# Performance work log

Hardware: AMD Instinct MI355X
Metric: run time of the kernel (lower is better)

Reference implementation:

```python
import jax, jax.numpy as jnp
import numpy as np

B, Q, T, H, V = 8, 1, 2048, 512, 32000


def setup_inputs() -> dict:
    key = jax.random.key(0)
    k0, k1, k2, k3, k4 = jax.random.split(key, 5)
    s1 = 1.0 / np.sqrt(2 * H)
    return {
        "input_embeds": jax.random.normal(k0, (B, Q, H), dtype=jnp.float32),
        "target_embeds": jax.random.normal(k1, (B, T, H), dtype=jnp.float32),
        "input_mask": jnp.ones((B, T), dtype=jnp.float32),
        # MLP params: l1 Linear(2H->H, bias), l2 Linear(H->1, no bias)
        "w1": (jax.random.normal(k2, (H, 2 * H), dtype=jnp.float32) * s1),
        "b1": jnp.zeros((H,), dtype=jnp.float32),
        "w2": (jax.random.normal(k3, (H,), dtype=jnp.float32) * (1.0 / np.sqrt(H))),
        # decoder: Linear(H->V, no bias) -> weight [V, H]
        "decoder_weight": (jax.random.normal(k4, (V, H), dtype=jnp.float32) * 0.02),
    }


def reference(input_embeds, target_embeds, input_mask, w1, b1, w2, decoder_weight):
    h = w1.shape[0]
    # l1(cat(q, t)) == q @ W1q^T + t @ W1t^T + b1  (split first linear)
    w1q, w1t = w1[:, :h], w1[:, h:]
    q_proj = jnp.einsum('bqh,kh->bqk', input_embeds, w1q)        # [B,Q,H]
    t_proj = jnp.einsum('bth,kh->btk', target_embeds, w1t)       # [B,T,H]
    # pairwise query x target MLP scoring
    ht = jax.nn.relu(q_proj[:, :, None, :] + t_proj[:, None, :, :] + b1)  # [B,Q,T,H]
    repair_logits = jnp.einsum('bqtk,k->bqt', ht, w2)             # [B,Q,T]
    # _mask: mask*logits - 1000*(1-mask); mask [B,T] -> [B,1,T]
    mask = input_mask[:, None, :]
    repair_logits = mask * repair_logits - 1000.0 * (1.0 - mask)
    # decoder branch: query x vocab-row MLP scoring
    d_proj = jnp.einsum('vh,kh->vk', decoder_weight, w1t)         # [V,H]
    hd = jax.nn.relu(q_proj[:, :, None, :] + d_proj[None, None, :, :] + b1)  # [B,Q,V,H]
    decoder_logits = jnp.einsum('bqvk,k->bqv', hd, w2)            # [B,Q,V]
    out = jnp.concatenate([decoder_logits, repair_logits], axis=2)  # [B,Q,V+T]
    return jnp.squeeze(out, axis=1)  # Q == 1 -> [B, V+T]
```

## Files before the change

kernel.cpp:

```cpp
#include <hip/hip_runtime.h>

#define Hdim 512
#define Bdim 8
#define Tdim 2048
#define Vdim 32000
#define OUTW (Vdim + Tdim)
#define DEC_TILES (Vdim / 128)
#define REP_TILES ((Bdim * Tdim) / 128)
#define NTILES (DEC_TILES + REP_TILES)
#define PROWS (Vdim + Bdim * Tdim)

typedef __attribute__((ext_vector_type(8))) short short8;
typedef __attribute__((ext_vector_type(16))) float f32x16;

__device__ __forceinline__ unsigned bfr(float f) {
    union { float f; unsigned u; } x; x.f = f;
    return (x.u + 0x7FFFu + ((x.u >> 16) & 1u)) >> 16;
}
__device__ __forceinline__ float lo16f(unsigned u) { return __uint_as_float(u << 16); }
__device__ __forceinline__ float hi16f(unsigned u) { return __uint_as_float(u & 0xffff0000u); }

#define N8_DEC (Vdim * Hdim / 8)
#define N8_TGT (Bdim * Tdim * Hdim / 8)
#define N8_W1  (Hdim * 1024 / 8)
#define N8_ALL (N8_DEC + N8_TGT + N8_W1)
#define CVT_BLOCKS (N8_ALL / 256)
#define QP_BLOCKS (Bdim * Hdim / 4)

__global__ __launch_bounds__(256) void prep_kernel(
    const float* __restrict__ dec, const float* __restrict__ tgt,
    const float* __restrict__ w1, const float* __restrict__ x,
    const float* __restrict__ b1,
    unsigned short* __restrict__ decbf, unsigned short* __restrict__ tgtbf,
    unsigned short* __restrict__ w1bf, float* __restrict__ qp)
{
    const int bid = blockIdx.x;
    if (bid < CVT_BLOCKS) {
        int i = bid * 256 + threadIdx.x;
        const float* src; unsigned short* dst; int j;
        if (i < N8_DEC)                { src = dec; dst = decbf; j = i; }
        else if (i < N8_DEC + N8_TGT)  { src = tgt; dst = tgtbf; j = i - N8_DEC; }
        else                           { src = w1;  dst = w1bf;  j = i - N8_DEC - N8_TGT; }
        const float4* s = (const float4*)src + (size_t)j * 2;
        float4 v0 = s[0], v1 = s[1];
        uint4 o;
        o.x = bfr(v0.x) | (bfr(v0.y) << 16);
        o.y = bfr(v0.z) | (bfr(v0.w) << 16);
        o.z = bfr(v1.x) | (bfr(v1.y) << 16);
        o.w = bfr(v1.z) | (bfr(v1.w) << 16);
        ((uint4*)dst)[j] = o;
    } else {
        const int widx = (bid - CVT_BLOCKS) * 4 + (threadIdx.x >> 6);
        const int lane = threadIdx.x & 63;
        const int b = widx >> 9, k = widx & 511;
        const float4* xr = (const float4*)(x + b * Hdim);
        const float4* wr = (const float4*)(w1 + (size_t)k * 1024);
        float4 x0 = xr[lane * 2], x1 = xr[lane * 2 + 1];
        float4 w0 = wr[lane * 2], w1v = wr[lane * 2 + 1];
        float s = x0.x * w0.x + x0.y * w0.y + x0.z * w0.z + x0.w * w0.w
                + x1.x * w1v.x + x1.y * w1v.y + x1.z * w1v.z + x1.w * w1v.w;
#pragma unroll
        for (int off = 32; off > 0; off >>= 1) s += __shfl_down(s, off);
        if (lane == 0) qp[b * Hdim + k] = s + b1[k];
    }
}

__global__ __launch_bounds__(256, 4) void gemm_kernel(
    const unsigned short* __restrict__ Adec,
    const unsigned short* __restrict__ Atgt,
    const unsigned short* __restrict__ Wbf,
    unsigned short* __restrict__ P)
{
    __shared__ struct { unsigned short A[128][64]; unsigned short W[128][64]; } u;

    const int tid  = threadIdx.x;
    const int lane = tid & 63;
    const int w    = tid >> 6;

    const int mt = blockIdx.x >> 2;
    const int n0 = (blockIdx.x & 3) << 7;
    const bool is_dec = (mt < DEC_TILES);
    const int m0 = (is_dec ? mt : mt - DEC_TILES) << 7;
    const unsigned short* __restrict__ A = is_dec ? Adec : Atgt;
    const int base = is_dec ? m0 : Vdim + m0;

    const int sr = lane >> 3;
    const int sc = (lane & 7) ^ sr;
    const unsigned short* gA = A   + (size_t)(m0 + w * 32 + sr) * 512  + sc * 8;
    const unsigned short* gW = Wbf + (size_t)(n0 + w * 32 + sr) * 1024 + 512 + sc * 8;

    f32x16 acc00, acc01, acc10, acc11;
#pragma unroll
    for (int i = 0; i < 16; ++i) { acc00[i] = 0.f; acc01[i] = 0.f; acc10[i] = 0.f; acc11[i] = 0.f; }

    const int wm  = (w & 1) << 6;
    const int wn  = (w >> 1) << 6;
    const int l31 = lane & 31;
    const int kh  = lane >> 5;

    for (int h0 = 0; h0 < Hdim; h0 += 64) {
        __syncthreads();
#pragma unroll
        for (int i = 0; i < 4; ++i) {
            __builtin_amdgcn_global_load_lds(
                (const __attribute__((address_space(1))) unsigned int*)(gA + i * 8 * 512),
                (__attribute__((address_space(3))) unsigned int*)(&u.A[w * 32 + i * 8][0]),
                16, 0, 0);
            __builtin_amdgcn_global_load_lds(
                (const __attribute__((address_space(1))) unsigned int*)(gW + i * 8 * 1024),
                (__attribute__((address_space(3))) unsigned int*)(&u.W[w * 32 + i * 8][0]),
                16, 0, 0);
        }
        gA += 64; gW += 64;
        __syncthreads();
#pragma unroll
        for (int s = 0; s < 4; ++s) {
            const int g  = s * 2 + kh;
            const int ca = ((g ^ (l31 & 7)) << 3);
            short8 a0 = *(const short8*)&u.A[wm + l31][ca];
            short8 a1 = *(const short8*)&u.A[wm + l31 + 32][ca];
            short8 b0 = *(const short8*)&u.W[wn + l31][ca];
            short8 b1 = *(const short8*)&u.W[wn + l31 + 32][ca];
            acc00 = __builtin_amdgcn_mfma_f32_32x32x16_bf16(a0, b0, acc00, 0, 0, 0);
            acc01 = __builtin_amdgcn_mfma_f32_32x32x16_bf16(a0, b1, acc01, 0, 0, 0);
            acc10 = __builtin_amdgcn_mfma_f32_32x32x16_bf16(a1, b0, acc10, 0, 0, 0);
            acc11 = __builtin_amdgcn_mfma_f32_32x32x16_bf16(a1, b1, acc11, 0, 0, 0);
        }
    }

#pragma unroll
    for (int r = 0; r < 16; ++r) {
        const int ra = (r & 3) + ((r >> 2) << 3) + (kh << 2);
        const size_t r0 = (size_t)(base + wm + ra) * 512 + n0;
        const size_t r1 = (size_t)(base + wm + 32 + ra) * 512 + n0;
        P[r0 + wn + l31]      = (unsigned short)bfr(acc00[r]);
        P[r0 + wn + 32 + l31] = (unsigned short)bfr(acc01[r]);
        P[r1 + wn + l31]      = (unsigned short)bfr(acc10[r]);
        P[r1 + wn + 32 + l31] = (unsigned short)bfr(acc11[r]);
    }
}

__global__ __launch_bounds__(256) void epi_kernel(
    const unsigned short* __restrict__ P, const float* __restrict__ qp,
    const float* __restrict__ w2, const float* __restrict__ mask,
    float* __restrict__ out)
{
    const int blk = blockIdx.x;
    const int tid = threadIdx.x;
    const int lane = tid & 63;
    const int wv = tid >> 6;
    const int c0 = lane * 8;
    const bool is_dec = (blk < DEC_TILES);

    const float4 w20 = *(const float4*)(w2 + c0);
    const float4 w21 = *(const float4*)(w2 + c0 + 4);

    if (is_dec) {
        const int row0 = blk * 128 + wv * 32;
        float4 q0[8], q1[8];
#pragma unroll
        for (int b = 0; b < 8; ++b) {
            q0[b] = *(const float4*)(qp + b * Hdim + c0);
            q1[b] = *(const float4*)(qp + b * Hdim + c0 + 4);
        }
        for (int i = 0; i < 32; ++i) {
            const uint4 pv = *(const uint4*)(P + (size_t)(row0 + i) * 512 + c0);
            float p[8];
            p[0] = lo16f(pv.x); p[1] = hi16f(pv.x);
            p[2] = lo16f(pv.y); p[3] = hi16f(pv.y);
            p[4] = lo16f(pv.z); p[5] = hi16f(pv.z);
            p[6] = lo16f(pv.w); p[7] = hi16f(pv.w);
            float s[8];
#pragma unroll
            for (int b = 0; b < 8; ++b) {
                float t;
                t  = fmaxf(p[0] + q0[b].x, 0.f) * w20.x;
                t += fmaxf(p[1] + q0[b].y, 0.f) * w20.y;
                t += fmaxf(p[2] + q0[b].z, 0.f) * w20.z;
                t += fmaxf(p[3] + q0[b].w, 0.f) * w20.w;
                t += fmaxf(p[4] + q1[b].x, 0.f) * w21.x;
                t += fmaxf(p[5] + q1[b].y, 0.f) * w21.y;
                t += fmaxf(p[6] + q1[b].z, 0.f) * w21.z;
                t += fmaxf(p[7] + q1[b].w, 0.f) * w21.w;
                s[b] = t;
            }
#pragma unroll
            for (int off = 32; off > 0; off >>= 1)
#pragma unroll
                for (int b = 0; b < 8; ++b) s[b] += __shfl_xor(s[b], off);
            if (lane == 0) {
#pragma unroll
                for (int b = 0; b < 8; ++b)
                    out[(size_t)b * OUTW + row0 + i] = s[b];
            }
        }
    } else {
        const int rl0 = (blk - DEC_TILES) * 128 + wv * 32;
        const int b = rl0 >> 11;
        const float4 q0 = *(const float4*)(qp + b * Hdim + c0);
        const float4 q1 = *(const float4*)(qp + b * Hdim + c0 + 4);
        for (int i = 0; i < 32; ++i) {
            const int rr = rl0 + i;
            const uint4 pv = *(const uint4*)(P + (size_t)(Vdim + rr) * 512 + c0);
            float p[8];
            p[0] = lo16f(pv.x); p[1] = hi16f(pv.x);
            p[2] = lo16f(pv.y); p[3] = hi16f(pv.y);
            p[4] = lo16f(pv.z); p[5] = hi16f(pv.z);
            p[6] = lo16f(pv.w); p[7] = hi16f(pv.w);
            float s;
            s  = fmaxf(p[0] + q0.x, 0.f) * w20.x;
            s += fmaxf(p[1] + q0.y, 0.f) * w20.y;
            s += fmaxf(p[2] + q0.z, 0.f) * w20.z;
            s += fmaxf(p[3] + q0.w, 0.f) * w20.w;
            s += fmaxf(p[4] + q1.x, 0.f) * w21.x;
            s += fmaxf(p[5] + q1.y, 0.f) * w21.y;
            s += fmaxf(p[6] + q1.z, 0.f) * w21.z;
            s += fmaxf(p[7] + q1.w, 0.f) * w21.w;
#pragma unroll
            for (int off = 32; off > 0; off >>= 1) s += __shfl_xor(s, off);
            if (lane == 0) {
                const int t = rr & 2047;
                const float mv = mask[b * Tdim + t];
                out[(size_t)b * OUTW + Vdim + t] = mv * s - 1000.f * (1.f - mv);
            }
        }
    }
}

extern "C" void kernel_launch(void* const* d_in, const int* in_sizes, int n_in,
                              void* d_out, int out_size, void* d_ws, size_t ws_size,
                              hipStream_t stream) {
    const float* input_embeds  = (const float*)d_in[0];
    const float* target_embeds = (const float*)d_in[1];
    const float* input_mask    = (const float*)d_in[2];
    const float* w1            = (const float*)d_in[3];
    const float* b1            = (const float*)d_in[4];
    const float* w2            = (const float*)d_in[5];
    const float* decoder_w     = (const float*)d_in[6];
    float* out = (float*)d_out;

    float* qp = (float*)d_ws;
    unsigned short* Pbuf  = (unsigned short*)((char*)d_ws + 16384);
    unsigned short* decbf = Pbuf + (size_t)PROWS * Hdim;
    unsigned short* tgtbf = decbf + (size_t)Vdim * Hdim;
    unsigned short* w1bf  = tgtbf + (size_t)Bdim * Tdim * Hdim;

    prep_kernel<<<CVT_BLOCKS + QP_BLOCKS, 256, 0, stream>>>(
        decoder_w, target_embeds, w1, input_embeds, b1, decbf, tgtbf, w1bf, qp);
    gemm_kernel<<<NTILES * 4, 256, 0, stream>>>(decbf, tgtbf, w1bf, Pbuf);
    epi_kernel<<<NTILES, 256, 0, stream>>>(Pbuf, qp, w2, input_mask, out);
}
```

Measured before the change: 215.2 us.

## Fuse fp32-to-bf16 conversion of activations into GEMM register-staged loads

The separate pass that converts the decoder weight and target embeddings to bf16 is removed. The GEMM now loads fp32 A tiles straight into registers, converts them to bf16 and writes swizzled LDS, with a register prefetch of the next K slice. Only the W1t slice is still pre-converted. Blocks are also reordered so the four N-chunks of each group of eight M-tiles run close together for L2 reuse of fp32 A, and the occupancy hint drops to 2 because of the added register pressure. This saves the bf16 write and reread of roughly 50M elements, but each A element is now read as fp32 four times, once per N-chunk.

```diff
diff --git a/kernel.cpp b/kernel.cpp
--- a/kernel.cpp
+++ b/kernel.cpp
@@ -1,4 +1,5 @@
 #include <hip/hip_runtime.h>
+#include <hip/hip_bf16.h>
 
 #define Hdim 512
 #define Bdim 8
@@ -17,40 +18,35 @@
     union { float f; unsigned u; } x; x.f = f;
     return (x.u + 0x7FFFu + ((x.u >> 16) & 1u)) >> 16;
 }
+__device__ __forceinline__ unsigned packbf2(float a, float b) {
+    __hip_bfloat162 h = __float22bfloat162_rn(make_float2(a, b));
+    union { __hip_bfloat162 h; unsigned u; } c; c.h = h;
+    return c.u;
+}
 __device__ __forceinline__ float lo16f(unsigned u) { return __uint_as_float(u << 16); }
 __device__ __forceinline__ float hi16f(unsigned u) { return __uint_as_float(u & 0xffff0000u); }
 
-#define N8_DEC (Vdim * Hdim / 8)
-#define N8_TGT (Bdim * Tdim * Hdim / 8)
-#define N8_W1  (Hdim * 1024 / 8)
-#define N8_ALL (N8_DEC + N8_TGT + N8_W1)
-#define CVT_BLOCKS (N8_ALL / 256)
+#define WT_BLOCKS 128
 #define QP_BLOCKS (Bdim * Hdim / 4)
 
 __global__ __launch_bounds__(256) void prep_kernel(
-    const float* __restrict__ dec, const float* __restrict__ tgt,
     const float* __restrict__ w1, const float* __restrict__ x,
     const float* __restrict__ b1,
-    unsigned short* __restrict__ decbf, unsigned short* __restrict__ tgtbf,
-    unsigned short* __restrict__ w1bf, float* __restrict__ qp)
+    unsigned short* __restrict__ wt, float* __restrict__ qp)
 {
     const int bid = blockIdx.x;
-    if (bid < CVT_BLOCKS) {
-        int i = bid * 256 + threadIdx.x;
-        const float* src; unsigned short* dst; int j;
-        if (i < N8_DEC)                { src = dec; dst = decbf; j = i; }
-        else if (i < N8_DEC + N8_TGT)  { src = tgt; dst = tgtbf; j = i - N8_DEC; }
-        else                           { src = w1;  dst = w1bf;  j = i - N8_DEC - N8_TGT; }
-        const float4* s = (const float4*)src + (size_t)j * 2;
-        float4 v0 = s[0], v1 = s[1];
+    if (bid < WT_BLOCKS) {
+        const int i = bid * 256 + threadIdx.x;
+        const int n = i >> 6;
+        const int kk = (i & 63) * 8;
+        const float4* s = (const float4*)(w1 + (size_t)n * 1024 + 512 + kk);
+        const float4 v0 = s[0], v1 = s[1];
         uint4 o;
-        o.x = bfr(v0.x) | (bfr(v0.y) << 16);
-        o.y = bfr(v0.z) | (bfr(v0.w) << 16);
-        o.z = bfr(v1.x) | (bfr(v1.y) << 16);
-        o.w = bfr(v1.z) | (bfr(v1.w) << 16);
-        ((uint4*)dst)[j] = o;
+        o.x = packbf2(v0.x, v0.y); o.y = packbf2(v0.z, v0.w);
+        o.z = packbf2(v1.x, v1.y); o.w = packbf2(v1.z, v1.w);
+        ((uint4*)wt)[i] = o;
     } else {
-        const int widx = (bid - CVT_BLOCKS) * 4 + (threadIdx.x >> 6);
+        const int widx = (bid - WT_BLOCKS) * 4 + (threadIdx.x >> 6);
         const int lane = threadIdx.x & 63;
         const int b = widx >> 9, k = widx & 511;
         const float4* xr = (const float4*)(x + b * Hdim);
@@ -65,10 +61,10 @@
     }
 }
 
-__global__ __launch_bounds__(256, 4) void gemm_kernel(
-    const unsigned short* __restrict__ Adec,
-    const unsigned short* __restrict__ Atgt,
-    const unsigned short* __restrict__ Wbf,
+__global__ __launch_bounds__(256, 2) void gemm_kernel(
+    const float* __restrict__ Adec,
+    const float* __restrict__ Atgt,
+    const unsigned short* __restrict__ Wt,
     unsigned short* __restrict__ P)
 {
     __shared__ struct { unsigned short A[128][64]; unsigned short W[128][64]; } u;
@@ -77,17 +73,23 @@
     const int lane = tid & 63;
     const int w    = tid >> 6;
 
-    const int mt = blockIdx.x >> 2;
-    const int n0 = (blockIdx.x & 3) << 7;
+    const int b = blockIdx.x;
+    const int mt = (b >> 5) * 8 + (b & 7);
+    if (mt >= NTILES) return;
+    const int chunk = (b >> 3) & 3;
+    const int n0 = chunk << 7;
     const bool is_dec = (mt < DEC_TILES);
     const int m0 = (is_dec ? mt : mt - DEC_TILES) << 7;
-    const unsigned short* __restrict__ A = is_dec ? Adec : Atgt;
+    const float* __restrict__ Af = is_dec ? Adec : Atgt;
     const int base = is_dec ? m0 : Vdim + m0;
 
-    const int sr = lane >> 3;
-    const int sc = (lane & 7) ^ sr;
-    const unsigned short* gA = A   + (size_t)(m0 + w * 32 + sr) * 512  + sc * 8;
-    const unsigned short* gW = Wbf + (size_t)(n0 + w * 32 + sr) * 1024 + 512 + sc * 8;
+    const int art = tid >> 4;
+    const int ac4 = tid & 15;
+    const int wrt = tid >> 3;
+    const int wgc = tid & 7;
+
+    const float4* gA = (const float4*)(Af + (size_t)(m0 + art) * 512) + ac4;
+    const uint4*  gW = (const uint4*)(Wt + (size_t)(n0 + wrt) * 512) + wgc;
 
     f32x16 acc00, acc01, acc10, acc11;
 #pragma unroll
@@ -98,21 +100,38 @@
     const int l31 = lane & 31;
     const int kh  = lane >> 5;
 
-    for (int h0 = 0; h0 < Hdim; h0 += 64) {
+    float4 ra[8];
+    uint4  rw[4];
+#pragma unroll
+    for (int p = 0; p < 8; ++p) ra[p] = gA[p * 2048];
+#pragma unroll
+    for (int p = 0; p < 4; ++p) rw[p] = gW[p * 2048];
+
+#pragma unroll
+    for (int h = 0; h < 8; ++h) {
         __syncthreads();
 #pragma unroll
-        for (int i = 0; i < 4; ++i) {
-            __builtin_amdgcn_global_load_lds(
-                (const __attribute__((address_space(1))) unsigned int*)(gA + i * 8 * 512),
-                (__attribute__((address_space(3))) unsigned int*)(&u.A[w * 32 + i * 8][0]),
-                16, 0, 0);
-            __builtin_amdgcn_global_load_lds(
-                (const __attribute__((address_space(1))) unsigned int*)(gW + i * 8 * 1024),
-                (__attribute__((address_space(3))) unsigned int*)(&u.W[w * 32 + i * 8][0]),
-                16, 0, 0);
-        }
-        gA += 64; gW += 64;
+        for (int p = 0; p < 8; ++p) {
+            const int r = p * 16 + art;
+            const int off = (((ac4 >> 1) ^ (r & 7)) << 3) + ((ac4 & 1) << 2);
+            uint2 v;
+            v.x = packbf2(ra[p].x, ra[p].y);
+            v.y = packbf2(ra[p].z, ra[p].w);
+            *(uint2*)&u.A[r][off] = v;
+        }
+#pragma unroll
+        for (int p = 0; p < 4; ++p) {
+            const int r = p * 32 + wrt;
+            const int off = ((wgc ^ (r & 7)) << 3);
+            *(uint4*)&u.W[r][off] = rw[p];
+        }
         __syncthreads();
+        if (h < 7) {
+#pragma unroll
+            for (int p = 0; p < 8; ++p) ra[p] = gA[p * 2048 + (h + 1) * 16];
+#pragma unroll
+            for (int p = 0; p < 4; ++p) rw[p] = gW[p * 2048 + (h + 1) * 8];
+        }
 #pragma unroll
         for (int s = 0; s < 4; ++s) {
             const int g  = s * 2 + kh;
@@ -130,9 +149,9 @@
 
 #pragma unroll
     for (int r = 0; r < 16; ++r) {
-        const int ra = (r & 3) + ((r >> 2) << 3) + (kh << 2);
-        const size_t r0 = (size_t)(base + wm + ra) * 512 + n0;
-        const size_t r1 = (size_t)(base + wm + 32 + ra) * 512 + n0;
+        const int ra2 = (r & 3) + ((r >> 2) << 3) + (kh << 2);
+        const size_t r0 = (size_t)(base + wm + ra2) * 512 + n0;
+        const size_t r1 = (size_t)(base + wm + 32 + ra2) * 512 + n0;
         P[r0 + wn + l31]      = (unsigned short)bfr(acc00[r]);
         P[r0 + wn + 32 + l31] = (unsigned short)bfr(acc01[r]);
         P[r1 + wn + l31]      = (unsigned short)bfr(acc10[r]);
@@ -240,13 +259,10 @@
     float* out = (float*)d_out;
 
     float* qp = (float*)d_ws;
-    unsigned short* Pbuf  = (unsigned short*)((char*)d_ws + 16384);
-    unsigned short* decbf = Pbuf + (size_t)PROWS * Hdim;
-    unsigned short* tgtbf = decbf + (size_t)Vdim * Hdim;
-    unsigned short* w1bf  = tgtbf + (size_t)Bdim * Tdim * Hdim;
-
-    prep_kernel<<<CVT_BLOCKS + QP_BLOCKS, 256, 0, stream>>>(
-        decoder_w, target_embeds, w1, input_embeds, b1, decbf, tgtbf, w1bf, qp);
-    gemm_kernel<<<NTILES * 4, 256, 0, stream>>>(decbf, tgtbf, w1bf, Pbuf);
+    unsigned short* Pbuf = (unsigned short*)((char*)d_ws + 16384);
+    unsigned short* wt   = Pbuf + (size_t)PROWS * Hdim;
+
+    prep_kernel<<<WT_BLOCKS + QP_BLOCKS, 256, 0, stream>>>(w1, input_embeds, b1, wt, qp);
+    gemm_kernel<<<48 * 32, 256, 0, stream>>>(decoder_w, target_embeds, wt, Pbuf);
     epi_kernel<<<NTILES, 256, 0, stream>>>(Pbuf, qp, w2, input_mask, out);
 }
```

Result: slower. 265.3 us (+23.3%).
